# Kernel optimization log

Measured on AMD Instinct MI355X. Metric: run time of the kernel, lower is better.

## Reference

```python
import jax, jax.numpy as jnp
import numpy as np

EPS = 1e-5

def layer_norm(x, gamma, beta):
    # biased variance (unbiased=False), matching torch code
    mean = jnp.mean(x, axis=-1, keepdims=True)
    var = jnp.mean((x - mean) ** 2, axis=-1, keepdims=True)
    return (x - mean) / jnp.sqrt(var + EPS) * gamma + beta

def setup_inputs() -> dict:
    key = jax.random.key(0)
    ks = jax.random.split(key, 8)
    B, T, C, H = 2, 2048, 768, 12
    Dff = 4 * C
    s = lambda n: 1.0 / np.sqrt(n)
    return {
        "x": jax.random.normal(ks[0], (B, T, C), dtype=jnp.float32),
        "mask": jnp.ones((B, T), dtype=jnp.int32),
        "Wqkv": jax.random.normal(ks[1], (C, 3 * C), dtype=jnp.float32) * s(C),
        "bqkv": jnp.zeros((3 * C,), dtype=jnp.float32),
        "Wp": jax.random.normal(ks[2], (C, C), dtype=jnp.float32) * s(C),
        "bp": jnp.zeros((C,), dtype=jnp.float32),
        "gamma1": jnp.ones((1, 1, C), dtype=jnp.float32),
        "beta1": jnp.zeros((1, 1, C), dtype=jnp.float32),
        "W1": jax.random.normal(ks[3], (C, Dff), dtype=jnp.float32) * s(C),
        "b1": jnp.zeros((Dff,), dtype=jnp.float32),
        "W2": jax.random.normal(ks[4], (Dff, C), dtype=jnp.float32) * s(Dff),
        "b2": jnp.zeros((C,), dtype=jnp.float32),
        "gamma2": jnp.ones((1, 1, C), dtype=jnp.float32),
        "beta2": jnp.zeros((1, 1, C), dtype=jnp.float32),
    }

def reference(x, mask, Wqkv, bqkv, Wp, bp, gamma1, beta1, W1, b1, W2, b2, gamma2, beta2):
    B, T, C = x.shape
    H = 12
    D = C // H
    # --- multi-head attention (hand-rolled QK^T-softmax-V) ---
    qkv = x @ Wqkv + bqkv                                  # (B,T,3C)
    q, k, v = jnp.split(qkv, 3, axis=-1)
    q = q.reshape(B, T, H, D).transpose(0, 2, 1, 3)        # (B,H,T,D)
    k = k.reshape(B, T, H, D).transpose(0, 2, 1, 3)
    v = v.reshape(B, T, H, D).transpose(0, 2, 1, 3)
    scores = jnp.einsum('bhtd,bhsd->bhts', q, k) * (D ** -0.5)  # (B,H,T,T)
    pad = (mask == 0)[:, None, None, :]                    # (B,1,1,T)
    scores = jnp.where(pad, -jnp.inf, scores)
    weights = jax.nn.softmax(scores, axis=-1)
    attn = jnp.einsum('bhts,bhsd->bhtd', weights, v)       # (B,H,T,D)
    attn = attn.transpose(0, 2, 1, 3).reshape(B, T, C)
    attn = attn @ Wp + bp
    # --- post-sublayer LN then residual (as in source) ---
    out = x + layer_norm(attn, gamma1, beta1)
    # --- MLP with exact GELU ---
    h = jax.nn.gelu(out @ W1 + b1, approximate=False)
    mlp = h @ W2 + b2
    out = out + layer_norm(mlp, gamma2, beta2)
    return out
```

## Files before the change

### kernel.cpp

```cpp
#include <hip/hip_runtime.h>
#include <math.h>

#define BB 2
#define TT 2048
#define CC 768
#define NH 12
#define HD 64
#define DFF 3072
#define MM (BB*TT)

typedef _Float16 f16;
typedef unsigned long long u64;
typedef unsigned int u32;
typedef __attribute__((ext_vector_type(8))) _Float16 f16x8;
typedef __attribute__((ext_vector_type(4))) _Float16 f16x4;
typedef __attribute__((ext_vector_type(4))) float f32x4;
typedef __attribute__((ext_vector_type(2))) unsigned int u32x2;
typedef __attribute__((ext_vector_type(4))) unsigned int u32x4;

#define QSCALE 0.18033688011112042f

#define GLD_LDS(gptr, lptr) \
  __builtin_amdgcn_global_load_lds((const __attribute__((address_space(1))) void*)(gptr), \
                                   (__attribute__((address_space(3))) void*)(lptr), 16, 0, 0)

#if __has_builtin(__builtin_amdgcn_exp2f)
#define EXP2(x) __builtin_amdgcn_exp2f(x)
#else
#define EXP2(x) exp2f(x)
#endif

#if __has_builtin(__builtin_amdgcn_rcpf)
#define RCP(x) __builtin_amdgcn_rcpf(x)
#else
#define RCP(x) (1.f / (x))
#endif

#if __has_builtin(__builtin_amdgcn_permlane32_swap) && __has_builtin(__builtin_amdgcn_permlane16_swap)
#define HAVE_PERMLANE_SWAP 1
#else
#define HAVE_PERMLANE_SWAP 0
#endif

__device__ __forceinline__ u32 pkrtz(float a, float b)
{
    auto h = __builtin_amdgcn_cvt_pkrtz(a, b);
    return __builtin_bit_cast(u32, h);
}

__device__ __forceinline__ float gelu_f(float x)
{
    const float y = fabsf(x) * 0.70710678118654752f;
    const float t = RCP(fmaf(0.3275911f, y, 1.f));
    float p = fmaf(1.061405429f, t, -1.453152027f);
    p = fmaf(p, t, 1.421413741f);
    p = fmaf(p, t, -0.284496736f);
    p = fmaf(p, t, 0.254829592f);
    p = p * t;
    const float e = EXP2(-y * y * 1.4426950408889634f);
    const float er = copysignf(1.f - p * e, x);
    return 0.5f * x * (1.f + er);
}

__device__ __forceinline__ void transpose_tile(const float* __restrict__ W,
                                               f16* __restrict__ Wt,
                                               int K, int N, int idx,
                                               float tile[32][33])
{
    const int kx = idx % (K / 32), ny = idx / (K / 32);
    const int k0 = kx * 32, n0 = ny * 32;
    const int r  = threadIdx.x >> 3;
    const int c4 = (threadIdx.x & 7) * 4;
    float4 v = *(const float4*)&W[(size_t)(k0 + r) * N + n0 + c4];
    tile[r][c4 + 0] = v.x; tile[r][c4 + 1] = v.y;
    tile[r][c4 + 2] = v.z; tile[r][c4 + 3] = v.w;
    __syncthreads();
    f16x4 o = {(f16)tile[c4 + 0][r], (f16)tile[c4 + 1][r],
               (f16)tile[c4 + 2][r], (f16)tile[c4 + 3][r]};
    *(f16x4*)&Wt[(size_t)(n0 + r) * K + k0 + c4] = o;
}

__global__ __launch_bounds__(256)
void conv_all(const float* __restrict__ x, f16* __restrict__ xh,
              const float* __restrict__ Wqkv, f16* __restrict__ Wqkvt,
              const float* __restrict__ Wp, f16* __restrict__ Wpt,
              const float* __restrict__ W1, f16* __restrict__ W1t,
              const float* __restrict__ W2, f16* __restrict__ W2t)
{
    __shared__ float tile[32][33];
    const int blk = blockIdx.x;
    if (blk < 3072) {
        const int i = blk * 256 + threadIdx.x;
        float4 v = ((const float4*)x)[i];
        f16x4 o = {(f16)v.x, (f16)v.y, (f16)v.z, (f16)v.w};
        ((f16x4*)xh)[i] = o;
    } else if (blk < 4800) {
        transpose_tile(Wqkv, Wqkvt, CC, 3 * CC, blk - 3072, tile);
    } else if (blk < 5376) {
        transpose_tile(Wp, Wpt, CC, CC, blk - 4800, tile);
    } else if (blk < 7680) {
        transpose_tile(W1, W1t, CC, DFF, blk - 5376, tile);
    } else {
        transpose_tile(W2, W2t, DFF, CC, blk - 7680, tile);
    }
}

template<int TM, int OUT_MODE, int GELU, int SPLITK, int AMODE, int MINW>
__global__ __launch_bounds__(256, MINW)
void gemm_mfma(const f16* __restrict__ A, const f16* __restrict__ Bt,
               const float* __restrict__ bias, void* __restrict__ Cout,
               f16* __restrict__ Kout, f16* __restrict__ Vout,
               const int* __restrict__ maskp, int M, int N, int K,
               const f16* __restrict__ Ao1,
               const float* __restrict__ lp0, const float* __restrict__ lp1)
{
    static_assert(TM == 64, "quad-buffer path is TM=64 only");
    constexpr int NT = 2;
    constexpr int G  = 512 / TM;
    __shared__ f16 As[4][TM * 32];
    __shared__ f16 Bs[4][128 * 32];

    int id = blockIdx.x;
    int kk = 0;
    if (SPLITK == 2) { kk = id & 1; id >>= 1; }
    const int xcd = id & 7, j = id >> 3;
    const int by = xcd * G + (j & (G - 1));
    const int bx = j / G;
    const int Keff = K / SPLITK;

    const int t = threadIdx.x;
    const int lane = t & 63, w = t >> 6;
    const int fr = lane & 15, quad = lane >> 4;
    const int row0 = by * TM, col0 = bx * 128;
    const int wn = w * 32;

    const int arow = w * (TM / 4) + (lane >> 2);
    const int brow = w * 32 + (lane >> 2);
    const int cg = (((lane & 3) ^ ((lane >> 3) & 3)) * 16);
    const char* ag = (const char*)(A  + (size_t)(row0 + arow) * K + kk * Keff) + cg;
    const char* bg = (const char*)(Bt + (size_t)(col0 + brow) * K + kk * Keff) + cg;
    const size_t rowK = (size_t)K * 2;
    const int wA = w * (TM / 4) * 32;
    const int wB = w * 32 * 32;
    const int sof = (quad ^ ((fr >> 1) & 3)) * 8;

    const f16 *a0p = nullptr, *a1p = nullptr;
    const float *lr0 = nullptr, *lr1 = nullptr;
    int lchunk8 = 0, aoff = 0;
    if (AMODE) {
        const int strow = lane >> 2, pchunk = lane & 3;
        lchunk8 = ((pchunk ^ ((lane >> 3) & 3))) * 8;
        const int ar = row0 + w * 16 + strow;
        a0p = A   + (size_t)ar * K + kk * Keff + lchunk8;
        a1p = Ao1 + (size_t)ar * K + kk * Keff + lchunk8;
        lr0 = lp0 + ar * NH;
        lr1 = lp1 + ar * NH;
        aoff = wA + strow * 32 + pchunk * 8;
    }

    f32x4 acc[4][NT] = {};

    if (AMODE) {
#pragma unroll
        for (int s = 0; s < 2; ++s) {
            f16x8 a0 = *(const f16x8*)(a0p + s * 32);
            f16x8 a1 = *(const f16x8*)(a1p + s * 32);
            const int hh = (kk * Keff + s * 32 + lchunk8) >> 6;
            const f16 lh = (f16)RCP(lr0[hh] + lr1[hh]);
            f16x8 sv;
#pragma unroll
            for (int jj = 0; jj < 8; ++jj) sv[jj] = (f16)((a0[jj] + a1[jj]) * lh);
            *(f16x8*)&As[s][aoff] = sv;
        }
    } else {
        GLD_LDS(ag, &As[0][wA]);
        GLD_LDS(ag + 64, &As[1][wA]);
    }
    GLD_LDS(bg, &Bs[0][wB]);
    GLD_LDS(bg + 16 * rowK, &Bs[0][wB + 16 * 32]);
    GLD_LDS(bg + 64, &Bs[1][wB]);
    GLD_LDS(bg + 64 + 16 * rowK, &Bs[1][wB + 16 * 32]);

    for (int k0 = 0; k0 < Keff; k0 += 64) {
        const int b0 = (k0 >> 5) & 3;
        const int b1 = (b0 + 1) & 3;
        f16x8 na00, na10, na01, na11;
        float nls0 = 1.f, nls1 = 1.f;
        if (AMODE && k0 + 64 < Keff) {
            na00 = *(const f16x8*)(a0p + k0 + 64);
            na10 = *(const f16x8*)(a1p + k0 + 64);
            na01 = *(const f16x8*)(a0p + k0 + 96);
            na11 = *(const f16x8*)(a1p + k0 + 96);
            const int h0 = (kk * Keff + k0 + 64 + lchunk8) >> 6;
            const int h1 = (kk * Keff + k0 + 96 + lchunk8) >> 6;
            nls0 = lr0[h0] + lr1[h0];
            nls1 = lr0[h1] + lr1[h1];
        }
        __syncthreads();
        if (k0 + 64 < Keff) {
            const int b2 = (b0 + 2) & 3, b3 = (b0 + 3) & 3;
            const size_t kb = (size_t)(k0 + 64) * 2;
            if (AMODE) {
                const f16 lh0 = (f16)RCP(nls0);
                f16x8 s0;
#pragma unroll
                for (int jj = 0; jj < 8; ++jj) s0[jj] = (f16)((na00[jj] + na10[jj]) * lh0);
                *(f16x8*)&As[b2][aoff] = s0;
                const f16 lh1 = (f16)RCP(nls1);
                f16x8 s1;
#pragma unroll
                for (int jj = 0; jj < 8; ++jj) s1[jj] = (f16)((na01[jj] + na11[jj]) * lh1);
                *(f16x8*)&As[b3][aoff] = s1;
            } else {
                GLD_LDS(ag + kb, &As[b2][wA]);
                GLD_LDS(ag + kb + 64, &As[b3][wA]);
            }
            GLD_LDS(bg + kb, &Bs[b2][wB]);
            GLD_LDS(bg + kb + 16 * rowK, &Bs[b2][wB + 16 * 32]);
            GLD_LDS(bg + kb + 64, &Bs[b3][wB]);
            GLD_LDS(bg + kb + 64 + 16 * rowK, &Bs[b3][wB + 16 * 32]);
        }
        {
            f16x8 af[4], bf[NT];
#pragma unroll
            for (int mt = 0; mt < 4; ++mt)
                af[mt] = *(const f16x8*)&As[b0][(mt * 16 + fr) * 32 + sof];
#pragma unroll
            for (int nt = 0; nt < NT; ++nt)
                bf[nt] = *(const f16x8*)&Bs[b0][(wn + nt * 16 + fr) * 32 + sof];
#pragma unroll
            for (int mt = 0; mt < 4; ++mt)
#pragma unroll
                for (int nt = 0; nt < NT; ++nt)
                    acc[mt][nt] = __builtin_amdgcn_mfma_f32_16x16x32_f16(
                        af[mt], bf[nt], acc[mt][nt], 0, 0, 0);
        }
        {
            f16x8 af[4], bf[NT];
#pragma unroll
            for (int mt = 0; mt < 4; ++mt)
                af[mt] = *(const f16x8*)&As[b1][(mt * 16 + fr) * 32 + sof];
#pragma unroll
            for (int nt = 0; nt < NT; ++nt)
                bf[nt] = *(const f16x8*)&Bs[b1][(wn + nt * 16 + fr) * 32 + sof];
#pragma unroll
            for (int mt = 0; mt < 4; ++mt)
#pragma unroll
                for (int nt = 0; nt < NT; ++nt)
                    acc[mt][nt] = __builtin_amdgcn_mfma_f32_16x16x32_f16(
                        af[mt], bf[nt], acc[mt][nt], 0, 0, 0);
        }
    }

    float bvs[NT];
#pragma unroll
    for (int nt = 0; nt < NT; ++nt)
        bvs[nt] = (SPLITK == 2 && kk) ? 0.f : bias[col0 + wn + nt * 16 + fr];
    f16* outbase = (f16*)Cout + (SPLITK == 2 ? (size_t)kk * M * N : 0);
#pragma unroll
    for (int mt = 0; mt < 4; ++mt) {
        const int rowb = row0 + mt * 16 + quad * 4;
        float mv[4] = {1.f, 1.f, 1.f, 1.f};
        if (OUT_MODE == 2 && col0 >= 1536) {
            int4 mi = *(const int4*)&maskp[rowb];
            mv[0] = mi.x ? 1.f : 0.f; mv[1] = mi.y ? 1.f : 0.f;
            mv[2] = mi.z ? 1.f : 0.f; mv[3] = mi.w ? 1.f : 0.f;
        }
#pragma unroll
        for (int nt = 0; nt < NT; ++nt) {
            const int col = col0 + wn + nt * 16 + fr;
            if (OUT_MODE == 2) {
                const int bq = rowb >> 11, sb = rowb & 2047;
                if (col0 < 768) {
#pragma unroll
                    for (int v = 0; v < 4; ++v)
                        ((f16*)Cout)[(size_t)(rowb + v) * 768 + col]
                            = (f16)((acc[mt][nt][v] + bvs[nt]) * QSCALE);
                } else if (col0 < 1536) {
                    const int dg = col - 768;
                    const int hh = dg >> 6, dd = dg & 63;
                    f16* kb = Kout + (size_t)(bq * NH + hh) * (TT * HD);
#pragma unroll
                    for (int v = 0; v < 4; ++v) {
                        const int s = sb + v;
                        kb[((s >> 4) * 128 + (dd >> 3) * 16 + (s & 15)) * 8 + (dd & 7)]
                            = (f16)(acc[mt][nt][v] + bvs[nt]);
                    }
                } else {
                    const int dg = col - 1536;
                    const int hh = dg >> 6, dd = dg & 63;
                    f16* vb = Vout + (size_t)(bq * NH + hh) * (TT * HD);
                    f16x4 pk = {(f16)((acc[mt][nt][0] + bvs[nt]) * mv[0]),
                                (f16)((acc[mt][nt][1] + bvs[nt]) * mv[1]),
                                (f16)((acc[mt][nt][2] + bvs[nt]) * mv[2]),
                                (f16)((acc[mt][nt][3] + bvs[nt]) * mv[3])};
                    *(f16x4*)&vb[((sb >> 3) * 64 + dd) * 8 + (sb & 7)] = pk;
                }
            } else {
#pragma unroll
                for (int v = 0; v < 4; ++v) {
                    float o = acc[mt][nt][v] + bvs[nt];
                    if (GELU) o = gelu_f(o);
                    outbase[(size_t)(rowb + v) * N + col] = (f16)o;
                }
            }
        }
    }
}

__global__ __launch_bounds__(256, 3)
void attn_mfma(const f16* __restrict__ qh, const f16* __restrict__ kth,
               const f16* __restrict__ vth, const int* __restrict__ mask,
               f16* __restrict__ O0, f16* __restrict__ O1,
               float* __restrict__ l0, float* __restrict__ l1)
{
    __shared__ __align__(16) char smem[16640];
    f16* Mf = (f16*)smem;
#if !HAVE_PERMLANE_SWAP
    f16* Ps = (f16*)(smem + 4096);
#endif
    float* Ored  = (float*)smem;
    float* lredp = (float*)(smem + 16384);

    const int id = blockIdx.x;
    const int xcd = id & 7, j = id >> 3;
    const int pair = xcd * 3 + j % 3;
    const int rem = j / 3;
    const int qt = rem >> 1, shalf = rem & 1;
    const int b = pair / NH, h = pair % NH;

    const int t = threadIdx.x, lane = t & 63, w = t >> 6;
    const int wq = w >> 1, ws = w & 1;
    const int fr = lane & 15, quad = lane >> 4;

    {
        int4 mi0 = *(const int4*)&mask[b * TT + t * 8];
        int4 mi1 = *(const int4*)&mask[b * TT + t * 8 + 4];
        f16x8 mrow;
        mrow[0] = mi0.x ? (f16)1.f : (f16)0.f; mrow[1] = mi0.y ? (f16)1.f : (f16)0.f;
        mrow[2] = mi0.z ? (f16)1.f : (f16)0.f; mrow[3] = mi0.w ? (f16)1.f : (f16)0.f;
        mrow[4] = mi1.x ? (f16)1.f : (f16)0.f; mrow[5] = mi1.y ? (f16)1.f : (f16)0.f;
        mrow[6] = mi1.z ? (f16)1.f : (f16)0.f; mrow[7] = mi1.w ? (f16)1.f : (f16)0.f;
        *(f16x8*)&Mf[t * 8] = mrow;
    }

    f16x8 qf[2][2];
#pragma unroll
    for (int nt = 0; nt < 2; ++nt)
#pragma unroll
        for (int ks = 0; ks < 2; ++ks)
            qf[nt][ks] = *(const f16x8*)&qh[(size_t)(b * TT + qt * 64 + wq * 32 + nt * 16 + fr) * CC
                                            + h * HD + ks * 32 + quad * 8];

    __syncthreads();

    const f16* KB = kth + (size_t)(b * NH + h) * (TT * HD);
    const f16* VB = vth + (size_t)(b * NH + h) * (TT * HD);
    int ko[2][2], vo[4];
#pragma unroll
    for (int mt = 0; mt < 2; ++mt)
#pragma unroll
        for (int ks = 0; ks < 2; ++ks)
            ko[mt][ks] = ((ws * 2 + mt) * 128 + (ks * 4 + quad) * 16 + fr) * 8;
#pragma unroll
    for (int nt = 0; nt < 4; ++nt)
        vo[nt] = ((ws * 4 + quad) * 64 + nt * 16 + fr) * 8;

    f32x4 oacc[2][4] = {};
    f32x4 lacc[2] = {};

    const int it0 = shalf * 16;
#pragma unroll 2
    for (int it = it0; it < it0 + 16; ++it) {
        const int ib = it * 4096;
        f16x8 vf[4];
#pragma unroll
        for (int nt = 0; nt < 4; ++nt)
            vf[nt] = *(const f16x8*)(VB + ib + vo[nt]);
        f16x8 kf[2][2];
#pragma unroll
        for (int mt = 0; mt < 2; ++mt)
#pragma unroll
            for (int ks = 0; ks < 2; ++ks)
                kf[mt][ks] = *(const f16x8*)(KB + ib + ko[mt][ks]);

        f32x4 sacc[2][2] = {};
        __builtin_amdgcn_s_setprio(1);
#pragma unroll
        for (int mt = 0; mt < 2; ++mt)
#pragma unroll
            for (int nt = 0; nt < 2; ++nt) {
                sacc[mt][nt] = __builtin_amdgcn_mfma_f32_16x16x32_f16(
                    kf[mt][0], qf[nt][0], sacc[mt][nt], 0, 0, 0);
                sacc[mt][nt] = __builtin_amdgcn_mfma_f32_16x16x32_f16(
                    kf[mt][1], qf[nt][1], sacc[mt][nt], 0, 0, 0);
            }
        __builtin_amdgcn_s_setprio(0);

        f16x8 mf = *(const f16x8*)&Mf[it * 64 + ws * 32 + quad * 8];

#if HAVE_PERMLANE_SWAP
#pragma unroll
        for (int nt = 0; nt < 2; ++nt) {
            const u32 pa = pkrtz(EXP2(sacc[0][nt][0]), EXP2(sacc[0][nt][1]));
            const u32 pb = pkrtz(EXP2(sacc[0][nt][2]), EXP2(sacc[0][nt][3]));
            const u32 pc = pkrtz(EXP2(sacc[1][nt][0]), EXP2(sacc[1][nt][1]));
            const u32 pd = pkrtz(EXP2(sacc[1][nt][2]), EXP2(sacc[1][nt][3]));
            const u32x2 e0 = __builtin_amdgcn_permlane32_swap(pa, pc, false, false);
            const u32x2 e1 = __builtin_amdgcn_permlane16_swap(e0.x, e0.y, false, false);
            const u32x2 e2 = __builtin_amdgcn_permlane32_swap(pb, pd, false, false);
            const u32x2 e3 = __builtin_amdgcn_permlane16_swap(e2.x, e2.y, false, false);
            const u32x4 pw = {e1.x, e3.x, e1.y, e3.y};
            const f16x8 pfr = __builtin_bit_cast(f16x8, pw);
            __builtin_amdgcn_s_setprio(1);
            lacc[nt] = __builtin_amdgcn_mfma_f32_16x16x32_f16(pfr, mf, lacc[nt], 0, 0, 0);
#pragma unroll
            for (int vt = 0; vt < 4; ++vt)
                oacc[nt][vt] = __builtin_amdgcn_mfma_f32_16x16x32_f16(
                    pfr, vf[vt], oacc[nt][vt], 0, 0, 0);
            __builtin_amdgcn_s_setprio(0);
        }
#else
#pragma unroll
        for (int mt = 0; mt < 2; ++mt)
#pragma unroll
            for (int nt = 0; nt < 2; ++nt) {
                f16x4 pk = {(f16)EXP2(sacc[mt][nt][0]), (f16)EXP2(sacc[mt][nt][1]),
                            (f16)EXP2(sacc[mt][nt][2]), (f16)EXP2(sacc[mt][nt][3])};
                *(f16x4*)&Ps[(wq * 32 + nt * 16 + fr) * 72 + ws * 32 + mt * 16 + quad * 4] = pk;
            }
        f16x8 pf[2];
#pragma unroll
        for (int mt = 0; mt < 2; ++mt)
            pf[mt] = *(const f16x8*)&Ps[(wq * 32 + mt * 16 + fr) * 72 + ws * 32 + quad * 8];
#pragma unroll
        for (int mt = 0; mt < 2; ++mt) {
            lacc[mt] = __builtin_amdgcn_mfma_f32_16x16x32_f16(pf[mt], mf, lacc[mt], 0, 0, 0);
#pragma unroll
            for (int nt = 0; nt < 4; ++nt)
                oacc[mt][nt] = __builtin_amdgcn_mfma_f32_16x16x32_f16(
                    pf[mt], vf[nt], oacc[mt][nt], 0, 0, 0);
        }
#endif
    }

    f16* Oout = shalf ? O1 : O0;
    float* lout = shalf ? l1 : l0;
    __syncthreads();
    if (ws == 1) {
#pragma unroll
        for (int mt = 0; mt < 2; ++mt) {
            const int q = wq * 32 + mt * 16 + quad * 4;
#pragma unroll
            for (int nt = 0; nt < 4; ++nt)
#pragma unroll
                for (int v = 0; v < 4; ++v)
                    Ored[(q + v) * 64 + nt * 16 + fr] = oacc[mt][nt][v];
            if (fr == 0)
#pragma unroll
                for (int v = 0; v < 4; ++v) lredp[q + v] = lacc[mt][v];
        }
    }
    __syncthreads();
    if (ws == 0) {
#pragma unroll
        for (int mt = 0; mt < 2; ++mt) {
            const int q0 = wq * 32 + mt * 16 + quad * 4;
            if (fr == 0)
#pragma unroll
                for (int v = 0; v < 4; ++v)
                    lout[(size_t)(b * TT + qt * 64 + q0 + v) * NH + h]
                        = lacc[mt][v] + lredp[q0 + v];
#pragma unroll
            for (int nt = 0; nt < 4; ++nt)
#pragma unroll
                for (int v = 0; v < 4; ++v) {
                    float o = oacc[mt][nt][v] + Ored[(q0 + v) * 64 + nt * 16 + fr];
                    Oout[(size_t)(b * TT + qt * 64 + q0 + v) * CC + h * HD + nt * 16 + fr]
                        = (f16)o;
                }
        }
    }
}

template<int WRITE_H>
__global__ __launch_bounds__(256)
void ln_residual(const float* __restrict__ res,
                 const f16* __restrict__ y0, const f16* __restrict__ y1,
                 const float* __restrict__ gamma, const float* __restrict__ beta,
                 float* __restrict__ outp, f16* __restrict__ outh)
{
    const int t = threadIdx.x;
    const int row = blockIdx.x * 8 + (t >> 5);
    const int c0 = (t & 31) * 24;
    const f16* yr0 = y0 + (size_t)row * CC + c0;
    const f16* yr1 = y1 + (size_t)row * CC + c0;
    float v[24];
    float s = 0.f, sq = 0.f;
#pragma unroll
    for (int i = 0; i < 3; ++i) {
        f16x8 a = *(const f16x8*)(yr0 + i * 8);
        f16x8 bb = *(const f16x8*)(yr1 + i * 8);
#pragma unroll
        for (int jj = 0; jj < 8; ++jj) {
            float vv = (float)a[jj] + (float)bb[jj];
            v[i * 8 + jj] = vv; s += vv; sq += vv * vv;
        }
    }
#pragma unroll
    for (int off = 1; off < 32; off <<= 1) {
        s  += __shfl_xor(s, off);
        sq += __shfl_xor(sq, off);
    }
    const float mean = s * (1.f / 768.f);
    const float var  = sq * (1.f / 768.f) - mean * mean;
    const float rstd = rsqrtf(var + 1e-5f);
    const float* rr = res + (size_t)row * CC + c0;
    float* orow = outp + (size_t)row * CC + c0;
#pragma unroll
    for (int i = 0; i < 6; ++i) {
        float4 r4 = *(const float4*)(rr + i * 4);
        float4 g4 = *(const float4*)(gamma + c0 + i * 4);
        float4 b4 = *(const float4*)(beta + c0 + i * 4);
        float4 o;
        o.x = r4.x + (v[i*4+0] - mean) * rstd * g4.x + b4.x;
        o.y = r4.y + (v[i*4+1] - mean) * rstd * g4.y + b4.y;
        o.z = r4.z + (v[i*4+2] - mean) * rstd * g4.z + b4.z;
        o.w = r4.w + (v[i*4+3] - mean) * rstd * g4.w + b4.w;
        *(float4*)(orow + i * 4) = o;
        if (WRITE_H) {
            f16x4 h4 = {(f16)o.x, (f16)o.y, (f16)o.z, (f16)o.w};
            *(f16x4*)(outh + (size_t)row * CC + c0 + i * 4) = h4;
        }
    }
}

extern "C" void kernel_launch(void* const* d_in, const int* in_sizes, int n_in,
                              void* d_out, int out_size, void* d_ws, size_t ws_size,
                              hipStream_t stream)
{
    const float* x     = (const float*)d_in[0];
    const int*   mask  = (const int*)  d_in[1];
    const float* Wqkv  = (const float*)d_in[2];
    const float* bqkv  = (const float*)d_in[3];
    const float* Wp    = (const float*)d_in[4];
    const float* bp    = (const float*)d_in[5];
    const float* g1    = (const float*)d_in[6];
    const float* be1   = (const float*)d_in[7];
    const float* W1    = (const float*)d_in[8];
    const float* b1    = (const float*)d_in[9];
    const float* W2    = (const float*)d_in[10];
    const float* b2    = (const float*)d_in[11];
    const float* g2    = (const float*)d_in[12];
    const float* be2   = (const float*)d_in[13];
    float* outp = (float*)d_out;

    char* wsb = (char*)d_ws;
    f16*   qhb    = (f16*)(wsb);
    f16*   kth    = (f16*)(wsb + 6291456);
    f16*   vth    = (f16*)(wsb + 12582912);
    f16*   O0     = (f16*)(wsb + 18874368);
    f16*   O1     = (f16*)(wsb + 25165824);
    f16*   hbuf   = (f16*)(wsb);
    f16*   xh     = (f16*)(wsb + 25165824);
    float* out1f  = (float*)(wsb + 25165824);
    f16*   Wqkvt  = (f16*)(wsb + 31457280);
    f16*   Wpt    = (f16*)(wsb + 34996224);
    f16*   W1t    = (f16*)(wsb + 37748736);
    f16*   W2t    = (f16*)(wsb + 42467328);
    f16*   p0     = (f16*)(wsb + 47185920);
    f16*   p1     = (f16*)(wsb + 53477376);
    f16*   out1h  = (f16*)(wsb + 59768832);
    float* l0     = (float*)(wsb + 66060288);
    float* l1     = (float*)(wsb + 66256896);

    const dim3 blk(256);

    conv_all<<<dim3(9984), blk, 0, stream>>>(x, xh, Wqkv, Wqkvt, Wp, Wpt,
                                             W1, W1t, W2, W2t);

    gemm_mfma<64, 2, 0, 1, 0, 3><<<dim3((3 * CC / 128) * (MM / 64)), blk, 0, stream>>>(
        xh, Wqkvt, bqkv, qhb, kth, vth, mask, MM, 3 * CC, CC,
        nullptr, nullptr, nullptr);
    attn_mfma<<<dim3((TT / 64) * NH * BB * 2), blk, 0, stream>>>(
        qhb, kth, vth, mask, O0, O1, l0, l1);
    gemm_mfma<64, 1, 0, 2, 1, 3><<<dim3(2 * (CC / 128) * (MM / 64)), blk, 0, stream>>>(
        O0, Wpt, bp, p0, nullptr, nullptr, nullptr, MM, CC, CC,
        O1, l0, l1);
    ln_residual<1><<<dim3(MM / 8), blk, 0, stream>>>(x, p0, p1, g1, be1, out1f, out1h);
    gemm_mfma<64, 1, 1, 1, 0, 3><<<dim3((DFF / 128) * (MM / 64)), blk, 0, stream>>>(
        out1h, W1t, b1, hbuf, nullptr, nullptr, nullptr, MM, DFF, CC,
        nullptr, nullptr, nullptr);
    gemm_mfma<64, 1, 0, 2, 0, 3><<<dim3(2 * (CC / 128) * (MM / 64)), blk, 0, stream>>>(
        hbuf, W2t, b2, p0, nullptr, nullptr, nullptr, MM, CC, DFF,
        nullptr, nullptr, nullptr);
    ln_residual<0><<<dim3(MM / 8), blk, 0, stream>>>(out1f, p0, p1, g2, be2, outp, nullptr);
}
```

Before: 265.9 us.

## Software-pipeline attention loop so next tile's QK^T overlaps current softmax-PV

In the permlane-swap path, the attention inner loop is restructured into a two-stage software pipeline. The QK^T MFMAs for the next key tile are issued before the exp/permlane/PV work of the current tile, with K prefetched one tile ahead. The aim is to hide transcendental and permute latency behind independent matrix ops. The cost is more live registers from double-buffered score accumulators and K fragments, which could lower occupancy. The fallback path also drops its setprio calls around QK^T.

```diff
diff --git a/kernel.cpp b/kernel.cpp
--- a/kernel.cpp
+++ b/kernel.cpp
@@ -370,6 +370,108 @@
     f32x4 lacc[2] = {};
 
     const int it0 = shalf * 16;
+
+#if HAVE_PERMLANE_SWAP
+#define SOFTMAX_PV(SACC, VF, MF)                                              \
+    {                                                                         \
+        _Pragma("unroll")                                                     \
+        for (int nt = 0; nt < 2; ++nt) {                                      \
+            const u32 pa = pkrtz(EXP2(SACC[0][nt][0]), EXP2(SACC[0][nt][1])); \
+            const u32 pb = pkrtz(EXP2(SACC[0][nt][2]), EXP2(SACC[0][nt][3])); \
+            const u32 pc = pkrtz(EXP2(SACC[1][nt][0]), EXP2(SACC[1][nt][1])); \
+            const u32 pd = pkrtz(EXP2(SACC[1][nt][2]), EXP2(SACC[1][nt][3])); \
+            const u32x2 e0 = __builtin_amdgcn_permlane32_swap(pa, pc, false, false); \
+            const u32x2 e1 = __builtin_amdgcn_permlane16_swap(e0.x, e0.y, false, false); \
+            const u32x2 e2 = __builtin_amdgcn_permlane32_swap(pb, pd, false, false); \
+            const u32x2 e3 = __builtin_amdgcn_permlane16_swap(e2.x, e2.y, false, false); \
+            const u32x4 pw = {e1.x, e3.x, e1.y, e3.y};                        \
+            const f16x8 pfr = __builtin_bit_cast(f16x8, pw);                  \
+            __builtin_amdgcn_s_setprio(1);                                    \
+            lacc[nt] = __builtin_amdgcn_mfma_f32_16x16x32_f16(pfr, MF, lacc[nt], 0, 0, 0); \
+            _Pragma("unroll")                                                 \
+            for (int vt = 0; vt < 4; ++vt)                                    \
+                oacc[nt][vt] = __builtin_amdgcn_mfma_f32_16x16x32_f16(        \
+                    pfr, VF[vt], oacc[nt][vt], 0, 0, 0);                      \
+            __builtin_amdgcn_s_setprio(0);                                    \
+        }                                                                     \
+    }
+
+    f16x8 kfA[2][2];
+#pragma unroll
+    for (int mt = 0; mt < 2; ++mt)
+#pragma unroll
+        for (int ks = 0; ks < 2; ++ks)
+            kfA[mt][ks] = *(const f16x8*)(KB + it0 * 4096 + ko[mt][ks]);
+    f32x4 saccA[2][2] = {};
+    __builtin_amdgcn_s_setprio(1);
+#pragma unroll
+    for (int mt = 0; mt < 2; ++mt)
+#pragma unroll
+        for (int nt = 0; nt < 2; ++nt) {
+            saccA[mt][nt] = __builtin_amdgcn_mfma_f32_16x16x32_f16(
+                kfA[mt][0], qf[nt][0], saccA[mt][nt], 0, 0, 0);
+            saccA[mt][nt] = __builtin_amdgcn_mfma_f32_16x16x32_f16(
+                kfA[mt][1], qf[nt][1], saccA[mt][nt], 0, 0, 0);
+        }
+    __builtin_amdgcn_s_setprio(0);
+
+    for (int it = it0; it < it0 + 16; it += 2) {
+        const int ibA = it * 4096, ibB = ibA + 4096, ibC = ibB + 4096;
+        f16x8 vfA[4];
+#pragma unroll
+        for (int nt = 0; nt < 4; ++nt)
+            vfA[nt] = *(const f16x8*)(VB + ibA + vo[nt]);
+        f16x8 kfB[2][2];
+#pragma unroll
+        for (int mt = 0; mt < 2; ++mt)
+#pragma unroll
+            for (int ks = 0; ks < 2; ++ks)
+                kfB[mt][ks] = *(const f16x8*)(KB + ibB + ko[mt][ks]);
+        f32x4 saccB[2][2] = {};
+        __builtin_amdgcn_s_setprio(1);
+#pragma unroll
+        for (int mt = 0; mt < 2; ++mt)
+#pragma unroll
+            for (int nt = 0; nt < 2; ++nt) {
+                saccB[mt][nt] = __builtin_amdgcn_mfma_f32_16x16x32_f16(
+                    kfB[mt][0], qf[nt][0], saccB[mt][nt], 0, 0, 0);
+                saccB[mt][nt] = __builtin_amdgcn_mfma_f32_16x16x32_f16(
+                    kfB[mt][1], qf[nt][1], saccB[mt][nt], 0, 0, 0);
+            }
+        __builtin_amdgcn_s_setprio(0);
+        const f16x8 mfA = *(const f16x8*)&Mf[it * 64 + ws * 32 + quad * 8];
+        SOFTMAX_PV(saccA, vfA, mfA)
+
+        f16x8 vfB[4];
+#pragma unroll
+        for (int nt = 0; nt < 4; ++nt)
+            vfB[nt] = *(const f16x8*)(VB + ibB + vo[nt]);
+#pragma unroll
+        for (int mt = 0; mt < 2; ++mt)
+#pragma unroll
+            for (int ks = 0; ks < 2; ++ks)
+                kfA[mt][ks] = *(const f16x8*)(KB + ibC + ko[mt][ks]);
+#pragma unroll
+        for (int mt = 0; mt < 2; ++mt)
+#pragma unroll
+            for (int nt = 0; nt < 2; ++nt)
+                saccA[mt][nt] = f32x4{0.f, 0.f, 0.f, 0.f};
+        __builtin_amdgcn_s_setprio(1);
+#pragma unroll
+        for (int mt = 0; mt < 2; ++mt)
+#pragma unroll
+            for (int nt = 0; nt < 2; ++nt) {
+                saccA[mt][nt] = __builtin_amdgcn_mfma_f32_16x16x32_f16(
+                    kfA[mt][0], qf[nt][0], saccA[mt][nt], 0, 0, 0);
+                saccA[mt][nt] = __builtin_amdgcn_mfma_f32_16x16x32_f16(
+                    kfA[mt][1], qf[nt][1], saccA[mt][nt], 0, 0, 0);
+            }
+        __builtin_amdgcn_s_setprio(0);
+        const f16x8 mfB = *(const f16x8*)&Mf[(it + 1) * 64 + ws * 32 + quad * 8];
+        SOFTMAX_PV(saccB, vfB, mfB)
+    }
+#undef SOFTMAX_PV
+#else
 #pragma unroll 2
     for (int it = it0; it < it0 + 16; ++it) {
         const int ib = it * 4096;
@@ -385,7 +487,6 @@
                 kf[mt][ks] = *(const f16x8*)(KB + ib + ko[mt][ks]);
 
         f32x4 sacc[2][2] = {};
-        __builtin_amdgcn_s_setprio(1);
 #pragma unroll
         for (int mt = 0; mt < 2; ++mt)
 #pragma unroll
@@ -395,32 +496,8 @@
                 sacc[mt][nt] = __builtin_amdgcn_mfma_f32_16x16x32_f16(
                     kf[mt][1], qf[nt][1], sacc[mt][nt], 0, 0, 0);
             }
-        __builtin_amdgcn_s_setprio(0);
 
         f16x8 mf = *(const f16x8*)&Mf[it * 64 + ws * 32 + quad * 8];
-
-#if HAVE_PERMLANE_SWAP
-#pragma unroll
-        for (int nt = 0; nt < 2; ++nt) {
-            const u32 pa = pkrtz(EXP2(sacc[0][nt][0]), EXP2(sacc[0][nt][1]));
-            const u32 pb = pkrtz(EXP2(sacc[0][nt][2]), EXP2(sacc[0][nt][3]));
-            const u32 pc = pkrtz(EXP2(sacc[1][nt][0]), EXP2(sacc[1][nt][1]));
-            const u32 pd = pkrtz(EXP2(sacc[1][nt][2]), EXP2(sacc[1][nt][3]));
-            const u32x2 e0 = __builtin_amdgcn_permlane32_swap(pa, pc, false, false);
-            const u32x2 e1 = __builtin_amdgcn_permlane16_swap(e0.x, e0.y, false, false);
-            const u32x2 e2 = __builtin_amdgcn_permlane32_swap(pb, pd, false, false);
-            const u32x2 e3 = __builtin_amdgcn_permlane16_swap(e2.x, e2.y, false, false);
-            const u32x4 pw = {e1.x, e3.x, e1.y, e3.y};
-            const f16x8 pfr = __builtin_bit_cast(f16x8, pw);
-            __builtin_amdgcn_s_setprio(1);
-            lacc[nt] = __builtin_amdgcn_mfma_f32_16x16x32_f16(pfr, mf, lacc[nt], 0, 0, 0);
-#pragma unroll
-            for (int vt = 0; vt < 4; ++vt)
-                oacc[nt][vt] = __builtin_amdgcn_mfma_f32_16x16x32_f16(
-                    pfr, vf[vt], oacc[nt][vt], 0, 0, 0);
-            __builtin_amdgcn_s_setprio(0);
-        }
-#else
 #pragma unroll
         for (int mt = 0; mt < 2; ++mt)
 #pragma unroll
@@ -441,8 +518,8 @@
                 oacc[mt][nt] = __builtin_amdgcn_mfma_f32_16x16x32_f16(
                     pf[mt], vf[nt], oacc[mt][nt], 0, 0, 0);
         }
+    }
 #endif
-    }
 
     f16* Oout = shalf ? O1 : O0;
     float* lout = shalf ? l1 : l0;
```

After: 271.2 us. Within noise of the previous version (+2.0%).
